# Kernel optimization log

Hardware: AMD Instinct MI355X
Metric: run time of the kernel (lower is better)

Reference implementation:

```python
import jax, jax.numpy as jnp
import numpy as np

NUM_HEADS = 12
NUM_BLOCKS = 12
EPS = 1e-5


def _layernorm(x, g, b):
    mu = jnp.mean(x, axis=-1, keepdims=True)
    var = jnp.mean(jnp.square(x - mu), axis=-1, keepdims=True)
    return (x - mu) * jax.lax.rsqrt(var + EPS) * g + b


def setup_inputs() -> dict:
    key = jax.random.key(0)
    ks = jax.random.split(key, 16)
    B, N, D, F = 4, 512, 768, 3072
    s = 1.0 / np.sqrt(D)
    sf = 1.0 / np.sqrt(F)
    return {
        "x": jax.random.normal(ks[0], (B, N, D), jnp.float32),
        "Wq": jax.random.normal(ks[1], (D, D), jnp.float32) * s,
        "bq": jnp.zeros((D,), jnp.float32),
        "Wk": jax.random.normal(ks[2], (D, D), jnp.float32) * s,
        "bk": jnp.zeros((D,), jnp.float32),
        "Wv": jax.random.normal(ks[3], (D, D), jnp.float32) * s,
        "bv": jnp.zeros((D,), jnp.float32),
        "g1": jnp.ones((D,), jnp.float32),
        "be1": jnp.zeros((D,), jnp.float32),
        "g2": jnp.ones((D,), jnp.float32),
        "be2": jnp.zeros((D,), jnp.float32),
        "W0": jax.random.normal(ks[4], (D, F), jnp.float32) * s,
        "b0": jnp.zeros((F,), jnp.float32),
        "W1": jax.random.normal(ks[5], (F, D), jnp.float32) * sf,
        "b1": jnp.zeros((D,), jnp.float32),
    }


def _attention(x, Wq, bq, Wk, bk, Wv, bv):
    B, N, D = x.shape
    H = NUM_HEADS
    hd = D // H
    q = (x @ Wq + bq).reshape(B, N, H, hd)
    k = (x @ Wk + bk).reshape(B, N, H, hd)
    v = (x @ Wv + bv).reshape(B, N, H, hd)
    # scores: [B, H, N, N], scaled by 1/sqrt(head_dim)
    scores = jnp.einsum("bqhd,bkhd->bhqk", q, k) / np.sqrt(hd)
    weights = jax.nn.softmax(scores, axis=-1)
    out = jnp.einsum("bhqk,bkhd->bqhd", weights, v)
    return out.reshape(B, N, D)


def reference(x, Wq, bq, Wk, bk, Wv, bv, g1, be1, g2, be2, W0, b0, W1, b1):
    # All blocks share the same weights (module appends the same block instance).
    for _ in range(NUM_BLOCKS):
        x = x + _attention(_layernorm(x, g1, be1), Wq, bq, Wk, bk, Wv, bv)
        h = _layernorm(x, g2, be2)
        h = jax.nn.gelu(h @ W0 + b0, approximate=False) @ W1 + b1
        x = x + h
    return x
```

## Files before the change

kernel.cpp:

```cpp
#include <hip/hip_runtime.h>
#include <stdint.h>

typedef float  f32x4  __attribute__((ext_vector_type(4)));
typedef __bf16 bf16x8 __attribute__((ext_vector_type(8)));

#define DEV __device__ __forceinline__

DEV short f2b(float f) {
    union { float f; unsigned u; } c; c.f = f;
    unsigned u = c.u;
    unsigned r = (u + 0x7fffu + ((u >> 16) & 1u)) >> 16;
    return (short)r;
}

DEV void gload_lds16(const void* g, void* l) {
    __builtin_amdgcn_global_load_lds(
        (const __attribute__((address_space(1))) void*)g,
        (__attribute__((address_space(3))) void*)l, 16, 0, 0);
}

template<int MODE, int NSPLIT>
DEV void gemm_body(
    const short* __restrict__ A, const short* __restrict__ Bt,
    const float* __restrict__ bias, const float* __restrict__ biask,
    const float* __restrict__ biasv,
    float* __restrict__ outf, short* __restrict__ o0,
    short* __restrict__ o1, short* __restrict__ o2,
    int M, int N, int K)
{
    constexpr int BM = 64, BN = 96, BK = 64;
    constexpr int FM = 2, FN = 3;
    __shared__ __align__(16) short As[2][BM * BK];
    __shared__ __align__(16) short Bs[2][BN * BK];

    const int tid  = threadIdx.x;
    const int w    = tid >> 6, lane = tid & 63;
    const int wr   = w >> 1,  wc   = w & 1;
    const int l16  = lane & 15, lhi = lane >> 4, sw = lane & 7;

    const int gx   = gridDim.x;
    const int nwg  = gx * gridDim.y;
    const int flat = blockIdx.y * gx + blockIdx.x;
    const int nf   = (flat & 7) * (nwg >> 3) + (flat >> 3);
    const int bx   = nf % gx, by = nf / gx;

    const int kz = (NSPLIT > 1) ? blockIdx.z : 0;

    const short* Ab = A  + (long)by * BM * K;
    const short* Bb = Bt + (long)bx * BN * K;

    const int ktPer = (K >> 6) / NSPLIT;
    const int ktBeg = kz * ktPer, ktEnd = ktBeg + ktPer;

    f32x4 acc[FM][FN];
#pragma unroll
    for (int m = 0; m < FM; ++m)
#pragma unroll
        for (int n = 0; n < FN; ++n) acc[m][n] = (f32x4)(0.0f);

    auto stage = [&](int buf, int kt) {
        const short* Ag = Ab + kt * BK;
#pragma unroll
        for (int i = 0; i < BM / 32; ++i) {
            int seg = i * 256 + tid;
            int row = seg >> 3;
            int gcs = (seg & 7) ^ (row & 7);
            gload_lds16(Ag + (long)row * K + gcs * 8, &As[buf][(i * 256 + w * 64) * 8]);
        }
        const short* Bg = Bb + kt * BK;
#pragma unroll
        for (int i = 0; i < BN / 32; ++i) {
            int seg = i * 256 + tid;
            int row = seg >> 3;
            int gcs = (seg & 7) ^ (row & 7);
            gload_lds16(Bg + (long)row * K + gcs * 8, &Bs[buf][(i * 256 + w * 64) * 8]);
        }
    };

    stage(0, ktBeg);
    asm volatile("s_waitcnt vmcnt(0)" ::: "memory");
    __builtin_amdgcn_s_barrier();

    int cur = 0;
    for (int kt = ktBeg; kt < ktEnd; ++kt) {
        if (kt + 1 < ktEnd) stage(cur ^ 1, kt + 1);
        const short* Ac = &As[cur][0];
        const short* Bc = &Bs[cur][0];
#pragma unroll
        for (int kk = 0; kk < 2; ++kk) {
            bf16x8 af[FM], bfr[FN];
#pragma unroll
            for (int m = 0; m < FM; ++m) {
                int ar = wr * 32 + m * 16 + l16;
                int ks = (kk * 4 + lhi) ^ sw;
                af[m] = *(const bf16x8*)(Ac + ar * BK + ks * 8);
            }
#pragma unroll
            for (int n = 0; n < FN; ++n) {
                int br = wc * 48 + n * 16 + l16;
                int ks = (kk * 4 + lhi) ^ sw;
                bfr[n] = *(const bf16x8*)(Bc + br * BK + ks * 8);
            }
#pragma unroll
            for (int m = 0; m < FM; ++m)
#pragma unroll
                for (int n = 0; n < FN; ++n)
                    acc[m][n] = __builtin_amdgcn_mfma_f32_16x16x32_bf16(
                        af[m], bfr[n], acc[m][n], 0, 0, 0);
        }
        asm volatile("s_waitcnt vmcnt(0)" ::: "memory");
        __builtin_amdgcn_s_barrier();
        cur ^= 1;
    }

    const int m0 = by * BM, n0 = bx * BN;
#pragma unroll
    for (int m = 0; m < FM; ++m) {
#pragma unroll
        for (int n = 0; n < FN; ++n) {
            const int grow0 = m0 + wr * 32 + m * 16 + lhi * 4;
            const int gcol  = n0 + wc * 48 + n * 16 + l16;
#pragma unroll
            for (int r = 0; r < 4; ++r) {
                float val = acc[m][n][r];
                int grow = grow0 + r;
                if constexpr (MODE == 1) {
                    int d  = gcol & 63;
                    int hh = gcol >> 6;
                    float bval = (hh < 12) ? bias[gcol]
                               : (hh < 24) ? biask[gcol - 768]
                                           : biasv[gcol - 1536];
                    float v = val + bval;
                    int bb = grow >> 9, s = grow & 511;
                    if (hh < 12) {
                        o0[((long)((bb * 12 + hh) * 512 + s) << 6) + d] = f2b(v * 0.125f);
                    } else if (hh < 24) {
                        o1[((long)((bb * 12 + (hh - 12)) * 512 + s) << 6) + d] = f2b(v);
                    } else {
                        o2[((long)((bb * 12 + (hh - 24)) * 64 + d) << 9) + s] = f2b(v);
                    }
                } else if constexpr (MODE == 2) {
                    float v = val + bias[gcol];
                    v = 0.5f * v * (1.0f + erff(v * 0.70710678118f));
                    o0[(long)grow * N + gcol] = f2b(v);
                } else {
                    outf[(long)kz * M * N + (long)grow * N + gcol] = val;
                }
            }
        }
    }
}

__global__ __launch_bounds__(256) void k_qkv(
    const short* A, const short* Bt,
    const float* bq, const float* bk, const float* bv,
    short* q, short* k, short* vt)
{ gemm_body<1, 1>(A, Bt, bq, bk, bv, nullptr, q, k, vt, 2048, 2304, 768); }

__global__ __launch_bounds__(256) void k_ffn1(
    const short* A, const short* Bt, const float* bias, short* h)
{ gemm_body<2, 1>(A, Bt, bias, nullptr, nullptr, nullptr, h, nullptr, nullptr, 2048, 3072, 768); }

__global__ __launch_bounds__(256) void k_ffn2(
    const short* A, const short* Bt, float* part)
{ gemm_body<3, 2>(A, Bt, nullptr, nullptr, nullptr, part, nullptr, nullptr, nullptr, 2048, 768, 3072); }

__global__ __launch_bounds__(256) void k_attn(
    const short* __restrict__ Qg,
    const short* __restrict__ Kg,
    const short* __restrict__ VTg,
    float* __restrict__ x)
{
    __shared__ __align__(16) short Qs[64 * 64];
    __shared__ __align__(16) short Ks[2][64 * 64];
    __shared__ __align__(16) short Vs[2][64 * 64];
    __shared__ __align__(16) short Ps[4][16 * 64];

    const int tid = threadIdx.x;
    const int w = tid >> 6, lane = tid & 63;
    const int l16 = lane & 15, lhi = lane >> 4;

    const int f  = blockIdx.y * 8 + blockIdx.x;
    const int nf = (f & 7) * 48 + (f >> 3);
    const int z  = nf >> 3, qt = nf & 7;
    const int q0 = qt * 64;

    const short* Qb = Qg  + (long)z * 512 * 64 + q0 * 64;
    const short* Kb = Kg  + (long)z * 512 * 64;
    const short* Vb = VTg + (long)z * 64 * 512;

    auto stageQ = [&]() {
#pragma unroll
        for (int i = 0; i < 2; ++i) {
            int seg = i * 256 + tid;
            int row = seg >> 3;
            int gc  = (seg & 7) ^ (row & 7);
            gload_lds16(Qb + row * 64 + gc * 8, Qs + (i * 256 + w * 64) * 8);
        }
    };
    auto stageK = [&](int buf, int kt) {
#pragma unroll
        for (int i = 0; i < 2; ++i) {
            int seg = i * 256 + tid;
            int row = seg >> 3;
            int gc  = (seg & 7) ^ (row & 7);
            gload_lds16(Kb + (kt * 64 + row) * 64 + gc * 8, &Ks[buf][(i * 256 + w * 64) * 8]);
        }
    };
    auto stageV = [&](int buf, int kt) {
#pragma unroll
        for (int i = 0; i < 2; ++i) {
            int seg = i * 256 + tid;
            int row = seg >> 3;
            int gc  = (seg & 7) ^ (row & 7);
            gload_lds16(Vb + (long)row * 512 + kt * 64 + gc * 8, &Vs[buf][(i * 256 + w * 64) * 8]);
        }
    };

    stageQ(); stageK(0, 0); stageV(0, 0);
    asm volatile("s_waitcnt vmcnt(0)" ::: "memory");
    __syncthreads();

    bf16x8 bq[2];
    {
        int qr = w * 16 + l16;
#pragma unroll
        for (int kk = 0; kk < 2; ++kk)
            bq[kk] = *(const bf16x8*)(Qs + qr * 64 + (((kk * 4 + lhi) ^ (l16 & 7)) * 8));
    }

    float l = 0.0f;
    f32x4 acc[4];
#pragma unroll
    for (int bn = 0; bn < 4; ++bn) acc[bn] = (f32x4)(0.0f);

    int cur = 0;
    for (int kt = 0; kt < 8; ++kt) {
        if (kt < 7) { stageK(cur ^ 1, kt + 1); stageV(cur ^ 1, kt + 1); }

        f32x4 s[4];
#pragma unroll
        for (int km = 0; km < 4; ++km) s[km] = (f32x4)(0.0f);
#pragma unroll
        for (int kk = 0; kk < 2; ++kk) {
#pragma unroll
            for (int km = 0; km < 4; ++km) {
                int kr = km * 16 + l16;
                bf16x8 ak = *(const bf16x8*)(&Ks[cur][kr * 64 + (((kk * 4 + lhi) ^ (l16 & 7)) * 8)]);
                s[km] = __builtin_amdgcn_mfma_f32_16x16x32_bf16(ak, bq[kk], s[km], 0, 0, 0);
            }
        }

        float p[16];
        float ts = 0.0f;
#pragma unroll
        for (int km = 0; km < 4; ++km)
#pragma unroll
            for (int r = 0; r < 4; ++r) {
                float e = __expf(s[km][r] - 8.0f);
                p[km * 4 + r] = e; ts += e;
            }
        ts += __shfl_xor(ts, 16);
        ts += __shfl_xor(ts, 32);
        l += ts;

        {
            short* Pw = &Ps[w][0];
#pragma unroll
            for (int km = 0; km < 4; ++km) {
                int g = km * 2 + (lhi >> 1);
                short4 pk;
                pk.x = f2b(p[km * 4 + 0]);
                pk.y = f2b(p[km * 4 + 1]);
                pk.z = f2b(p[km * 4 + 2]);
                pk.w = f2b(p[km * 4 + 3]);
                *(short4*)(Pw + l16 * 64 + ((g ^ (l16 & 7)) * 8) + (lhi & 1) * 4) = pk;
            }
        }

#pragma unroll
        for (int kk = 0; kk < 2; ++kk) {
            bf16x8 ap = *(const bf16x8*)(&Ps[w][l16 * 64 + (((kk * 4 + lhi) ^ (l16 & 7)) * 8)]);
#pragma unroll
            for (int bn = 0; bn < 4; ++bn) {
                int vr = bn * 16 + l16;
                bf16x8 bv = *(const bf16x8*)(&Vs[cur][vr * 64 + (((kk * 4 + lhi) ^ (l16 & 7)) * 8)]);
                acc[bn] = __builtin_amdgcn_mfma_f32_16x16x32_bf16(ap, bv, acc[bn], 0, 0, 0);
            }
        }

        asm volatile("s_waitcnt vmcnt(0)" ::: "memory");
        __builtin_amdgcn_s_barrier();
        cur ^= 1;
    }

    float inv = 1.0f / l;
    float invr[4];
#pragma unroll
    for (int r = 0; r < 4; ++r) invr[r] = __shfl(inv, lhi * 4 + r);
    const int zb = z / 12, zh = z - (z / 12) * 12;
#pragma unroll
    for (int bn = 0; bn < 4; ++bn)
#pragma unroll
        for (int r = 0; r < 4; ++r) {
            long idx = ((long)(zb * 512 + q0 + w * 16 + lhi * 4 + r)) * 768 + zh * 64 + bn * 16 + l16;
            x[idx] += acc[bn][r] * invr[r];
        }
}

__global__ __launch_bounds__(256) void k_ln(
    const float* __restrict__ x, const float* __restrict__ g,
    const float* __restrict__ be, short* __restrict__ out)
{
    int row  = blockIdx.x * 4 + (threadIdx.x >> 6);
    int lane = threadIdx.x & 63;
    const float4* xr = (const float4*)(x + (long)row * 768);
    float4 v0 = xr[lane], v1 = xr[lane + 64], v2 = xr[lane + 128];
    float f[12] = {v0.x, v0.y, v0.z, v0.w, v1.x, v1.y, v1.z, v1.w, v2.x, v2.y, v2.z, v2.w};

    float s = 0.f;
#pragma unroll
    for (int j = 0; j < 12; ++j) s += f[j];
#pragma unroll
    for (int o = 32; o; o >>= 1) s += __shfl_xor(s, o);
    float mu = s * (1.0f / 768.0f);
    float s2 = 0.f;
#pragma unroll
    for (int j = 0; j < 12; ++j) { f[j] -= mu; s2 += f[j] * f[j]; }
#pragma unroll
    for (int o = 32; o; o >>= 1) s2 += __shfl_xor(s2, o);
    float rstd = rsqrtf(s2 * (1.0f / 768.0f) + 1e-5f);

    const float4* gr = (const float4*)g;
    const float4* br = (const float4*)be;
    short4* orow = (short4*)(out + (long)row * 768);
#pragma unroll
    for (int jb = 0; jb < 3; ++jb) {
        float4 gg = gr[lane + 64 * jb], bb = br[lane + 64 * jb];
        short4 o4;
        o4.x = f2b(f[4 * jb + 0] * rstd * gg.x + bb.x);
        o4.y = f2b(f[4 * jb + 1] * rstd * gg.y + bb.y);
        o4.z = f2b(f[4 * jb + 2] * rstd * gg.z + bb.z);
        o4.w = f2b(f[4 * jb + 3] * rstd * gg.w + bb.w);
        orow[lane + 64 * jb] = o4;
    }
}

template<int DO_LN>
__global__ __launch_bounds__(256) void k_redln(
    const float* __restrict__ part, const float* __restrict__ bias,
    float* __restrict__ x, const float* __restrict__ g,
    const float* __restrict__ be, short* __restrict__ out)
{
    int row  = blockIdx.x * 4 + (threadIdx.x >> 6);
    int lane = threadIdx.x & 63;
    const float4* p0 = (const float4*)part + (long)row * 192;
    const float4* p1 = (const float4*)(part + 2048l * 768) + (long)row * 192;
    const float4* b4 = (const float4*)bias;
    float4* xr = (float4*)(x + (long)row * 768);

    float f[12];
#pragma unroll
    for (int jb = 0; jb < 3; ++jb) {
        int idx = lane + 64 * jb;
        float4 a = p0[idx], b = p1[idx], c = b4[idx], xv = xr[idx];
        xv.x += a.x + b.x + c.x;
        xv.y += a.y + b.y + c.y;
        xv.z += a.z + b.z + c.z;
        xv.w += a.w + b.w + c.w;
        xr[idx] = xv;
        f[4 * jb + 0] = xv.x; f[4 * jb + 1] = xv.y;
        f[4 * jb + 2] = xv.z; f[4 * jb + 3] = xv.w;
    }

    if constexpr (DO_LN) {
        float s = 0.f;
#pragma unroll
        for (int j = 0; j < 12; ++j) s += f[j];
#pragma unroll
        for (int o = 32; o; o >>= 1) s += __shfl_xor(s, o);
        float mu = s * (1.0f / 768.0f);
        float s2 = 0.f;
#pragma unroll
        for (int j = 0; j < 12; ++j) { f[j] -= mu; s2 += f[j] * f[j]; }
#pragma unroll
        for (int o = 32; o; o >>= 1) s2 += __shfl_xor(s2, o);
        float rstd = rsqrtf(s2 * (1.0f / 768.0f) + 1e-5f);

        const float4* gr = (const float4*)g;
        const float4* br = (const float4*)be;
        short4* orow = (short4*)(out + (long)row * 768);
#pragma unroll
        for (int jb = 0; jb < 3; ++jb) {
            float4 gg = gr[lane + 64 * jb], bb = br[lane + 64 * jb];
            short4 o4;
            o4.x = f2b(f[4 * jb + 0] * rstd * gg.x + bb.x);
            o4.y = f2b(f[4 * jb + 1] * rstd * gg.y + bb.y);
            o4.z = f2b(f[4 * jb + 2] * rstd * gg.z + bb.z);
            o4.w = f2b(f[4 * jb + 3] * rstd * gg.w + bb.w);
            orow[lane + 64 * jb] = o4;
        }
    }
}

__global__ __launch_bounds__(256) void transpose_w(
    const float* __restrict__ in, short* __restrict__ out, int R, int C)
{
    __shared__ float t[32][33];
    int r0 = blockIdx.y * 32, c0 = blockIdx.x * 32;
    int tx = threadIdx.x & 31, ty = threadIdx.x >> 5;
#pragma unroll
    for (int p = 0; p < 4; ++p)
        t[ty + 8 * p][tx] = in[(long)(r0 + ty + 8 * p) * C + c0 + tx];
    __syncthreads();
#pragma unroll
    for (int p = 0; p < 4; ++p)
        out[(long)(c0 + ty + 8 * p) * R + r0 + tx] = f2b(t[tx][ty + 8 * p]);
}

__global__ __launch_bounds__(256) void transpose_w3(
    const float* __restrict__ Wq, const float* __restrict__ Wk,
    const float* __restrict__ Wv, short* __restrict__ out)
{
    const float* in = (blockIdx.z == 0) ? Wq : (blockIdx.z == 1) ? Wk : Wv;
    short* o = out + (long)blockIdx.z * 768 * 768;
    __shared__ float t[32][33];
    int r0 = blockIdx.y * 32, c0 = blockIdx.x * 32;
    int tx = threadIdx.x & 31, ty = threadIdx.x >> 5;
#pragma unroll
    for (int p = 0; p < 4; ++p)
        t[ty + 8 * p][tx] = in[(long)(r0 + ty + 8 * p) * 768 + c0 + tx];
    __syncthreads();
#pragma unroll
    for (int p = 0; p < 4; ++p)
        o[(long)(c0 + ty + 8 * p) * 768 + r0 + tx] = f2b(t[tx][ty + 8 * p]);
}

extern "C" void kernel_launch(void* const* d_in, const int* in_sizes, int n_in,
                              void* d_out, int out_size, void* d_ws, size_t ws_size,
                              hipStream_t stream)
{
    (void)in_sizes; (void)n_in; (void)out_size; (void)ws_size;
    const float* x_in = (const float*)d_in[0];
    const float* Wq  = (const float*)d_in[1];
    const float* bq  = (const float*)d_in[2];
    const float* Wk  = (const float*)d_in[3];
    const float* bk  = (const float*)d_in[4];
    const float* Wv  = (const float*)d_in[5];
    const float* bv  = (const float*)d_in[6];
    const float* g1  = (const float*)d_in[7];
    const float* be1 = (const float*)d_in[8];
    const float* g2  = (const float*)d_in[9];
    const float* be2 = (const float*)d_in[10];
    const float* W0  = (const float*)d_in[11];
    const float* b0  = (const float*)d_in[12];
    const float* W1  = (const float*)d_in[13];
    const float* b1  = (const float*)d_in[14];

    float* x = (float*)d_out;

    char* ws = (char*)d_ws;
    size_t off = 0;
    auto alloc = [&](size_t bytes) -> char* {
        char* p = ws + off; off = (off + bytes + 255) & ~(size_t)255; return p;
    };
    short* wqkvt = (short*)alloc(2304l * 768 * 2);
    short* w0t   = (short*)alloc(3072l * 768 * 2);
    short* w1t   = (short*)alloc(768l * 3072 * 2);
    short* lnb   = (short*)alloc(2048l * 768 * 2);
    short* q     = (short*)alloc(2048l * 768 * 2);
    short* k     = (short*)alloc(2048l * 768 * 2);
    short* vt    = (short*)alloc(2048l * 768 * 2);
    short* h     = (short*)alloc(2048l * 3072 * 2);
    float* part  = (float*)alloc(2l * 2048 * 768 * 4);

    hipMemcpyAsync(x, x_in, 2048l * 768 * 4, hipMemcpyDeviceToDevice, stream);

    transpose_w3<<<dim3(24, 24, 3), 256, 0, stream>>>(Wq, Wk, Wv, wqkvt);
    transpose_w<<<dim3(96, 24), 256, 0, stream>>>(W0, w0t, 768, 3072);
    transpose_w<<<dim3(24, 96), 256, 0, stream>>>(W1, w1t, 3072, 768);

    for (int it = 0; it < 12; ++it) {
        if (it == 0)
            k_ln<<<512, 256, 0, stream>>>(x, g1, be1, lnb);
        k_qkv<<<dim3(24, 32), 256, 0, stream>>>(lnb, wqkvt, bq, bk, bv, q, k, vt);
        k_attn<<<dim3(8, 48), 256, 0, stream>>>(q, k, vt, x);
        k_ln<<<512, 256, 0, stream>>>(x, g2, be2, lnb);
        k_ffn1<<<dim3(32, 32), 256, 0, stream>>>(lnb, w0t, b0, h);
        k_ffn2<<<dim3(8, 32, 2), 256, 0, stream>>>(h, w1t, part);
        if (it < 11)
            k_redln<1><<<512, 256, 0, stream>>>(part, b1, x, g1, be1, lnb);
        else
            k_redln<0><<<512, 256, 0, stream>>>(part, b1, x, nullptr, nullptr, nullptr);
    }
}
```

Baseline: 1.009 ms.

## Raise FFN2 split-K to four and use column-major tile order for QKV/FFN1

The FFN2 GEMM now splits K four ways instead of two, giving 1024 workgroups instead of 512 for better CU occupancy. The reduce+layernorm kernel sums four partial planes to match. QKV and FFN1 switch tile rasterization to column-major, so consecutive workgroups share weight tiles, aiming for better L2 reuse. In exchange, the partial buffer doubles and the reduction reads twice as much fp32 data.

New measurement: 1.066 ms. +5.7%, slower.

```diff
diff --git a/kernel.cpp b/kernel.cpp
--- a/kernel.cpp
+++ b/kernel.cpp
@@ -19,7 +19,7 @@
         (__attribute__((address_space(3))) void*)l, 16, 0, 0);
 }
 
-template<int MODE, int NSPLIT>
+template<int MODE, int NSPLIT, int CM>
 DEV void gemm_body(
     const short* __restrict__ A, const short* __restrict__ Bt,
     const float* __restrict__ bias, const float* __restrict__ biask,
@@ -38,11 +38,13 @@
     const int wr   = w >> 1,  wc   = w & 1;
     const int l16  = lane & 15, lhi = lane >> 4, sw = lane & 7;
 
-    const int gx   = gridDim.x;
-    const int nwg  = gx * gridDim.y;
+    const int gx   = gridDim.x, gy = gridDim.y;
+    const int nwg  = gx * gy;
     const int flat = blockIdx.y * gx + blockIdx.x;
     const int nf   = (flat & 7) * (nwg >> 3) + (flat >> 3);
-    const int bx   = nf % gx, by = nf / gx;
+    int bx, by;
+    if constexpr (CM) { bx = nf / gy; by = nf - bx * gy; }
+    else              { bx = nf % gx; by = nf / gx; }
 
     const int kz = (NSPLIT > 1) ? blockIdx.z : 0;
 
@@ -155,15 +157,15 @@
     const short* A, const short* Bt,
     const float* bq, const float* bk, const float* bv,
     short* q, short* k, short* vt)
-{ gemm_body<1, 1>(A, Bt, bq, bk, bv, nullptr, q, k, vt, 2048, 2304, 768); }
+{ gemm_body<1, 1, 1>(A, Bt, bq, bk, bv, nullptr, q, k, vt, 2048, 2304, 768); }
 
 __global__ __launch_bounds__(256) void k_ffn1(
     const short* A, const short* Bt, const float* bias, short* h)
-{ gemm_body<2, 1>(A, Bt, bias, nullptr, nullptr, nullptr, h, nullptr, nullptr, 2048, 3072, 768); }
+{ gemm_body<2, 1, 1>(A, Bt, bias, nullptr, nullptr, nullptr, h, nullptr, nullptr, 2048, 3072, 768); }
 
 __global__ __launch_bounds__(256) void k_ffn2(
     const short* A, const short* Bt, float* part)
-{ gemm_body<3, 2>(A, Bt, nullptr, nullptr, nullptr, part, nullptr, nullptr, nullptr, 2048, 768, 3072); }
+{ gemm_body<3, 4, 0>(A, Bt, nullptr, nullptr, nullptr, part, nullptr, nullptr, nullptr, 2048, 768, 3072); }
 
 __global__ __launch_bounds__(256) void k_attn(
     const short* __restrict__ Qg,
@@ -354,8 +356,11 @@
 {
     int row  = blockIdx.x * 4 + (threadIdx.x >> 6);
     int lane = threadIdx.x & 63;
+    const long plane = 2048l * 768 / 4;
     const float4* p0 = (const float4*)part + (long)row * 192;
-    const float4* p1 = (const float4*)(part + 2048l * 768) + (long)row * 192;
+    const float4* p1 = p0 + plane;
+    const float4* p2 = p1 + plane;
+    const float4* p3 = p2 + plane;
     const float4* b4 = (const float4*)bias;
     float4* xr = (float4*)(x + (long)row * 768);
 
@@ -363,11 +368,12 @@
 #pragma unroll
     for (int jb = 0; jb < 3; ++jb) {
         int idx = lane + 64 * jb;
-        float4 a = p0[idx], b = p1[idx], c = b4[idx], xv = xr[idx];
-        xv.x += a.x + b.x + c.x;
-        xv.y += a.y + b.y + c.y;
-        xv.z += a.z + b.z + c.z;
-        xv.w += a.w + b.w + c.w;
+        float4 a = p0[idx], b = p1[idx], c2 = p2[idx], d = p3[idx];
+        float4 c = b4[idx], xv = xr[idx];
+        xv.x += a.x + b.x + c2.x + d.x + c.x;
+        xv.y += a.y + b.y + c2.y + d.y + c.y;
+        xv.z += a.z + b.z + c2.z + d.z + c.z;
+        xv.w += a.w + b.w + c2.w + d.w + c.w;
         xr[idx] = xv;
         f[4 * jb + 0] = xv.x; f[4 * jb + 1] = xv.y;
         f[4 * jb + 2] = xv.z; f[4 * jb + 3] = xv.w;
@@ -472,7 +478,7 @@
     short* k     = (short*)alloc(2048l * 768 * 2);
     short* vt    = (short*)alloc(2048l * 768 * 2);
     short* h     = (short*)alloc(2048l * 3072 * 2);
-    float* part  = (float*)alloc(2l * 2048 * 768 * 4);
+    float* part  = (float*)alloc(4l * 2048 * 768 * 4);
 
     hipMemcpyAsync(x, x_in, 2048l * 768 * 4, hipMemcpyDeviceToDevice, stream);
 
@@ -487,7 +493,7 @@
         k_attn<<<dim3(8, 48), 256, 0, stream>>>(q, k, vt, x);
         k_ln<<<512, 256, 0, stream>>>(x, g2, be2, lnb);
         k_ffn1<<<dim3(32, 32), 256, 0, stream>>>(lnb, w0t, b0, h);
-        k_ffn2<<<dim3(8, 32, 2), 256, 0, stream>>>(h, w1t, part);
+        k_ffn2<<<dim3(8, 32, 4), 256, 0, stream>>>(h, w1t, part);
         if (it < 11)
             k_redln<1><<<512, 256, 0, stream>>>(part, b1, x, g1, be1, lnb);
         else
```
